# Kernel optimization log

Hardware: AMD Instinct MI355X
Metric: run time of the kernel (lower is better)

## Reference

```python
import jax, jax.numpy as jnp
import numpy as np
from jax import lax

DIVISOR = 2.0

def setup_inputs() -> dict:
    key = jax.random.key(0)
    k1, k2, k3, k4 = jax.random.split(key, 4)
    x = jax.random.normal(k1, (32, 3, 32, 128, 128), dtype=jnp.float16)
    conv_w = jax.random.normal(k2, (16, 3, 3, 3, 3), dtype=jnp.float16) * 0.1
    conv_b = jax.random.normal(k3, (16,), dtype=jnp.float16)
    bias = jax.random.normal(k4, (16,), dtype=jnp.float16)
    return {"x": x, "conv_w": conv_w, "conv_b": conv_b, "bias": bias}

def reference(x, conv_w, conv_b, bias):
    # Conv3d (valid padding, stride 1), fp16 like conv.half()
    y = lax.conv_general_dilated(
        x, conv_w, window_strides=(1, 1, 1), padding="VALID",
        dimension_numbers=("NCDHW", "OIDHW", "NCDHW"))
    y = y + conv_b[None, :, None, None, None]
    # Fused ReLU + 2x2x2 max pool
    y = jnp.maximum(y, jnp.asarray(0, y.dtype))
    B, C, D, H, W = y.shape
    Dp, Hp, Wp = D // 2, H // 2, W // 2
    pooled = y[:, :, :2 * Dp, :2 * Hp, :2 * Wp].reshape(
        B, C, Dp, 2, Hp, 2, Wp, 2).max(axis=(3, 5, 7))  # [B,C,Dp,Hp,Wp]
    # Spatial mean in fp32 (kernel accumulates in float)
    avg = pooled.astype(jnp.float32).mean(axis=(2, 3, 4))  # [B,C]
    # /divisor + bias[c], then sum over channels -> [B,1,1,1]
    per_ch = avg / DIVISOR + bias.astype(jnp.float32)[None, :]
    return per_ch.sum(axis=1).reshape(B, 1, 1, 1)
```

## Files before the change

kernel.cpp:

```cpp
#include <hip/hip_runtime.h>
#include <hip/hip_bf16.h>


typedef __attribute__((ext_vector_type(8)))  short  short8;
typedef __attribute__((ext_vector_type(2)))  float  floatx2;
typedef __attribute__((ext_vector_type(4)))  float  floatx4;
typedef __attribute__((ext_vector_type(16))) float  floatx16;

__device__ __forceinline__ short f2bf(float f) {
    unsigned u = __builtin_bit_cast(unsigned, f);
    unsigned r = (u + 0x7FFFu + ((u >> 16) & 1u)) >> 16;
    return (short)r;
}

__device__ __forceinline__ unsigned pkbf2(float a, float b) {
    __hip_bfloat162 h = __float22bfloat162_rn(float2{a, b});
    unsigned r;
    __builtin_memcpy(&r, &h, 4);
    return r;
}

template <int CTRL>
__device__ __forceinline__ float dpp_max(float v) {
    int x = __builtin_bit_cast(int, v);
    int y = __builtin_amdgcn_mov_dpp(x, CTRL, 0xF, 0xF, true);
    return fmaxf(v, __builtin_bit_cast(float, y));
}

#define BAR() asm volatile("s_waitcnt lgkmcnt(0)\n\ts_barrier" ::: "memory")

#define BUFSZ 16640

__global__ void init_kernel(const float* __restrict__ wg,
                            const float* __restrict__ biasg,
                            short* __restrict__ wtab,
                            float* __restrict__ out)
{
    const int t = threadIdx.x;
    if (t < 576) {
        const int lane = t & 63, f = t >> 6;
        const int kh = f / 3, kw = f % 3;
        const int m = lane & 31, hs = lane >> 5;
        const int ch = m >> 1, dd = m & 1;
        short8 v;
        #pragma unroll
        for (int j = 0; j < 8; ++j) {
            const int s = hs * 8 + j;
            const int dl = s >> 2, ci = s & 3;
            const int kd = dl - dd;
            v[j] = (ci < 3 && kd >= 0 && kd < 3)
                 ? f2bf(wg[ch * 81 + ci * 27 + kd * 9 + kh * 3 + kw]) : (short)0;
        }
        ((short8*)wtab)[f * 64 + lane] = v;
    }
    if (t < 32) {
        float s = 0.f;
        #pragma unroll
        for (int cc = 0; cc < 16; ++cc) s += biasg[cc];
        out[t] = s;
    }
}

__global__ __launch_bounds__(512, 4) void fused_conv_pool_reduce(
    const float* __restrict__ xg,
    const short* __restrict__ wtab,
    const float* __restrict__ cbg,
    float* __restrict__ out)
{
    __shared__ __align__(16) short rawT[2 * 130 * 64];
    __shared__ float wsums[8];

    const int lin = blockIdx.y * 63 + blockIdx.x;
    const int nl  = (lin & 7) * 252 + (lin >> 3);
    const int hp  = nl % 63;
    const int b   = nl / 63;

    const int tid = threadIdx.x;
    const int lane = tid & 63;
    const int wv   = tid >> 6;
    const int hs   = lane >> 5;

    short8 af[9];
    #pragma unroll
    for (int f = 0; f < 9; ++f) af[f] = ((const short8*)wtab)[f * 64 + lane];
    const float cbv = cbg[(lane >> 1) & 15];
    float maskA[4];
    #pragma unroll
    for (int a = 0; a < 4; ++a) {
        const bool ok = ((lane & 1) == 0) && (wv * 8 + 2 * a + hs <= 62);
        maskA[a] = ok ? 1.0f : 0.0f;
    }

    if (tid < 64)
        *(unsigned long long*)((char*)rawT + (tid >> 5) * BUFSZ + 16384 + (tid & 31) * 8) = 0ULL;

    #define SWZ(r) (((r) ^ ((r) >> 3)) & 7)

    const int w4 = tid & 31, dr2 = (tid >> 5) & 1, rr = (tid >> 6) & 1, hr2 = (tid >> 7) & 3;
    int waddr2[2];
    #pragma unroll
    for (int j = 0; j < 2; ++j) {
        const int row = 2 * w4 + 64 * rr + j;
        waddr2[j] = row * 128 + ((hr2 * 2) ^ SWZ(row)) * 16 + dr2 * 8;
    }

    const int wi = (lane >> 1) & 15, hh = lane & 1;
    int raddr[3][3];
    #pragma unroll
    for (int kh = 0; kh < 3; ++kh) {
        #pragma unroll
        for (int kw = 0; kw < 3; ++kw) {
            const int row = wv * 16 + wi + kw;
            const int phys = ((hh + kh) * 2 + hs) ^ SWZ(row);
            raddr[kh][kw] = row * 128 + phys * 16;
        }
    }

    {
        const int w4p = tid & 31, drp = (tid >> 5) & 3, hrp = (tid >> 7) & 3;
        const float* srcP = xg + ((size_t)b * 96 + drp) * 16384 + (2 * hp + hrp) * 128 + 4 * w4p;
        const floatx4 c0 = *(const floatx4*)(srcP);
        const floatx4 c1 = *(const floatx4*)(srcP + 524288);
        const floatx4 c2 = *(const floatx4*)(srcP + 1048576);
        const int chunkL = hrp * 2 + (drp >> 1);
        #pragma unroll
        for (int i = 0; i < 4; ++i) {
            const int row = 4 * w4p + i;
            const int ad = row * 128 + (chunkL ^ SWZ(row)) * 16 + (drp & 1) * 8;
            uint2 pk;
            pk.x = pkbf2(c0[i], c1[i]);
            pk.y = pkbf2(c2[i], 0.0f);
            *(uint2*)((char*)rawT + ad) = pk;
        }
    }

    const float* src2 = xg + ((size_t)b * 96 + 4 + dr2) * 16384
                      + (2 * hp + hr2) * 128 + 2 * w4 + 64 * rr;
    floatx2 A0 = *(const floatx2*)(src2);
    floatx2 A1 = *(const floatx2*)(src2 + 524288);
    floatx2 A2 = *(const floatx2*)(src2 + 1048576);

    float vsum = 0.f;
    for (int dp = 0; dp < 15; ++dp) {
        const int p16 = (dp & 1) << 4;
        if (dp <= 13) {
            const int bw = (((dp >> 1) + 1) & 1) * BUFSZ;
            uint2 pk0, pk1;
            pk0.x = pkbf2(A0[0], A1[0]); pk0.y = pkbf2(A2[0], 0.0f);
            pk1.x = pkbf2(A0[1], A1[1]); pk1.y = pkbf2(A2[1], 0.0f);
            *(uint2*)((char*)rawT + bw + (waddr2[0] ^ p16)) = pk0;
            *(uint2*)((char*)rawT + bw + (waddr2[1] ^ p16)) = pk1;
            if (dp <= 12) {
                src2 += 32768;
                A0 = *(const floatx2*)(src2);
                A1 = *(const floatx2*)(src2 + 524288);
                A2 = *(const floatx2*)(src2 + 1048576);
            }
        }
        BAR();

        const int roff = (((dp + hs) >> 1) & 1) * BUFSZ;

        floatx16 acc = {0.f,0.f,0.f,0.f,0.f,0.f,0.f,0.f,
                        0.f,0.f,0.f,0.f,0.f,0.f,0.f,0.f};
        #pragma unroll
        for (int kh = 0; kh < 3; ++kh) {
            #pragma unroll
            for (int kw = 0; kw < 3; ++kw) {
                const short8 bf = *(const short8*)((char*)rawT + roff + (raddr[kh][kw] ^ p16));
                acc = __builtin_amdgcn_mfma_f32_32x32x16_bf16(bf, af[kh * 3 + kw], acc, 0, 0, 0);
            }
        }
        #pragma unroll
        for (int a = 0; a < 4; ++a) {
            float m01 = fmaxf(acc[4 * a],     acc[4 * a + 1]);
            float m23 = fmaxf(acc[4 * a + 2], acc[4 * a + 3]);
            float m   = fmaxf(m01, m23);
            m = dpp_max<0xB1>(m);
            const float v = fmaxf(m + cbv, 0.f);
            vsum = fmaf(maskA[a], v, vsum);
        }
    }

    float s = vsum;
    #pragma unroll
    for (int off = 1; off < 64; off <<= 1) s += __shfl_xor(s, off, 64);

    if (lane == 0) wsums[wv] = s;
    __syncthreads();
    if (tid == 0) {
        float bs = 0.f;
        #pragma unroll
        for (int i = 0; i < 8; ++i) bs += wsums[i];
        atomicAdd(&out[b], bs * (1.0f / 119070.0f));
    }
}

extern "C" void kernel_launch(void* const* d_in, const int* in_sizes, int n_in,
                              void* d_out, int out_size, void* d_ws, size_t ws_size,
                              hipStream_t stream) {
    const float* x      = (const float*)d_in[0];
    const float* conv_w = (const float*)d_in[1];
    const float* conv_b = (const float*)d_in[2];
    const float* bias   = (const float*)d_in[3];
    float* out = (float*)d_out;
    short* wtab = (short*)d_ws;

    init_kernel<<<1, 576, 0, stream>>>(conv_w, bias, wtab, out);
    dim3 grid(63, 32);
    fused_conv_pool_reduce<<<grid, 512, 0, stream>>>(x, wtab, conv_b, out);
}
```

Baseline: 287.2 us.

## Split conv-pool blocks into single-wave workgroups with barrier-free 4-slot LDS ring

Each 512-thread block that covered a whole output row is replaced by 64-thread single-wave blocks, each handling one 16-wide W segment, so the grid grows eightfold. Each wave loads its own input halo into a private 4-slot LDS ring. This removes the per-depth-step s_barrier and the cross-wave shared reduction, and each wave atomically adds its partial sum to the output directly. It also raises wave priority around the MFMA chain. The cost is redundant halo loads, scalar rather than vector global loads, and eight times more atomics. Visibility of LDS writes within a single wave now relies on implicit ordering and compiler waitcnt insertion.

```diff
diff --git a/kernel.cpp b/kernel.cpp
--- a/kernel.cpp
+++ b/kernel.cpp
@@ -3,8 +3,6 @@
 
 
 typedef __attribute__((ext_vector_type(8)))  short  short8;
-typedef __attribute__((ext_vector_type(2)))  float  floatx2;
-typedef __attribute__((ext_vector_type(4)))  float  floatx4;
 typedef __attribute__((ext_vector_type(16))) float  floatx16;
 
 __device__ __forceinline__ short f2bf(float f) {
@@ -27,9 +25,7 @@
     return fmaxf(v, __builtin_bit_cast(float, y));
 }
 
-#define BAR() asm volatile("s_waitcnt lgkmcnt(0)\n\ts_barrier" ::: "memory")
-
-#define BUFSZ 16640
+#define SLOTSZ 1152
 
 __global__ void init_kernel(const float* __restrict__ wg,
                             const float* __restrict__ biasg,
@@ -61,23 +57,23 @@
     }
 }
 
-__global__ __launch_bounds__(512, 4) void fused_conv_pool_reduce(
+__global__ __launch_bounds__(64, 4) void fused_conv_pool_reduce(
     const float* __restrict__ xg,
     const short* __restrict__ wtab,
     const float* __restrict__ cbg,
     float* __restrict__ out)
 {
-    __shared__ __align__(16) short rawT[2 * 130 * 64];
-    __shared__ float wsums[8];
+    __shared__ __align__(16) short slots[4 * 18 * 32];
 
-    const int lin = blockIdx.y * 63 + blockIdx.x;
-    const int nl  = (lin & 7) * 252 + (lin >> 3);
-    const int hp  = nl % 63;
-    const int b   = nl / 63;
+    const int lin  = blockIdx.y * 63 + blockIdx.x;
+    const int nl   = (lin & 7) * 2016 + (lin >> 3);
+    const int hp   = nl % 63;
+    const int rest = nl / 63;
+    const int wv   = rest & 7;
+    const int b    = rest >> 3;
+    const int wbase = wv * 16;
 
-    const int tid = threadIdx.x;
-    const int lane = tid & 63;
-    const int wv   = tid >> 6;
+    const int lane = threadIdx.x;
     const int hs   = lane >> 5;
 
     short8 af[9];
@@ -87,90 +83,82 @@
     float maskA[4];
     #pragma unroll
     for (int a = 0; a < 4; ++a) {
-        const bool ok = ((lane & 1) == 0) && (wv * 8 + 2 * a + hs <= 62);
+        const bool ok = ((lane & 1) == 0) && (8 * wv + 2 * a + hs <= 62);
         maskA[a] = ok ? 1.0f : 0.0f;
     }
 
-    if (tid < 64)
-        *(unsigned long long*)((char*)rawT + (tid >> 5) * BUFSZ + 16384 + (tid & 31) * 8) = 0ULL;
-
-    #define SWZ(r) (((r) ^ ((r) >> 3)) & 7)
-
-    const int w4 = tid & 31, dr2 = (tid >> 5) & 1, rr = (tid >> 6) & 1, hr2 = (tid >> 7) & 3;
-    int waddr2[2];
-    #pragma unroll
-    for (int j = 0; j < 2; ++j) {
-        const int row = 2 * w4 + 64 * rr + j;
-        waddr2[j] = row * 128 + ((hr2 * 2) ^ SWZ(row)) * 16 + dr2 * 8;
-    }
+    const int rowA = lane & 15, hlA = lane >> 4;
+    const int wadA = rowA * 64 + ((hlA ^ (rowA & 3)) * 16);
+    const float* gA = xg + (size_t)b * 1572864 + (2 * hp + hlA) * 128 + wbase + rowA;
+    const bool doB = (lane < 8);
+    const bool wv7 = (wv == 7);
+    const int rowB = 16 + (lane & 1), hlB = (lane >> 1) & 3;
+    const int wadB = rowB * 64 + ((hlB ^ (rowB & 3)) * 16);
+    const float* gB = xg + (size_t)b * 1572864 + (2 * hp + hlB) * 128 + wbase + rowB;
 
     const int wi = (lane >> 1) & 15, hh = lane & 1;
-    int raddr[3][3];
+    int rad[3][3];
     #pragma unroll
     for (int kh = 0; kh < 3; ++kh) {
         #pragma unroll
         for (int kw = 0; kw < 3; ++kw) {
-            const int row = wv * 16 + wi + kw;
-            const int phys = ((hh + kh) * 2 + hs) ^ SWZ(row);
-            raddr[kh][kw] = row * 128 + phys * 16;
+            const int row = wi + kw;
+            rad[kh][kw] = row * 64 + (((hh + kh) ^ (row & 3)) * 16);
         }
     }
 
-    {
-        const int w4p = tid & 31, drp = (tid >> 5) & 3, hrp = (tid >> 7) & 3;
-        const float* srcP = xg + ((size_t)b * 96 + drp) * 16384 + (2 * hp + hrp) * 128 + 4 * w4p;
-        const floatx4 c0 = *(const floatx4*)(srcP);
-        const floatx4 c1 = *(const floatx4*)(srcP + 524288);
-        const floatx4 c2 = *(const floatx4*)(srcP + 1048576);
-        const int chunkL = hrp * 2 + (drp >> 1);
-        #pragma unroll
-        for (int i = 0; i < 4; ++i) {
-            const int row = 4 * w4p + i;
-            const int ad = row * 128 + (chunkL ^ SWZ(row)) * 16 + (drp & 1) * 8;
-            uint2 pk;
-            pk.x = pkbf2(c0[i], c1[i]);
-            pk.y = pkbf2(c2[i], 0.0f);
-            *(uint2*)((char*)rawT + ad) = pk;
+    float A0,A1,A2,A3,A4,A5, B0=0.f,B1=0.f,B2=0.f,B3=0.f,B4=0.f,B5=0.f;
+    auto loadPair = [&](int p) {
+        const float* pa = gA + (size_t)(2 * p) * 16384;
+        A0 = pa[0];      A1 = pa[524288];  A2 = pa[1048576];
+        A3 = pa[16384];  A4 = pa[540672];  A5 = pa[1064960];
+        if (doB) {
+            if (!wv7) {
+                const float* pb = gB + (size_t)(2 * p) * 16384;
+                B0 = pb[0];     B1 = pb[524288]; B2 = pb[1048576];
+                B3 = pb[16384]; B4 = pb[540672]; B5 = pb[1064960];
+            } else {
+                B0 = B1 = B2 = B3 = B4 = B5 = 0.f;
+            }
         }
-    }
+    };
+    auto writePair = [&](int sbase) {
+        uint4 q;
+        q.x = pkbf2(A0, A1);  q.y = pkbf2(A2, 0.f);
+        q.z = pkbf2(A3, A4);  q.w = pkbf2(A5, 0.f);
+        *(uint4*)((char*)slots + sbase + wadA) = q;
+        if (doB) {
+            uint4 r;
+            r.x = pkbf2(B0, B1);  r.y = pkbf2(B2, 0.f);
+            r.z = pkbf2(B3, B4);  r.w = pkbf2(B5, 0.f);
+            *(uint4*)((char*)slots + sbase + wadB) = r;
+        }
+    };
 
-    const float* src2 = xg + ((size_t)b * 96 + 4 + dr2) * 16384
-                      + (2 * hp + hr2) * 128 + 2 * w4 + 64 * rr;
-    floatx2 A0 = *(const floatx2*)(src2);
-    floatx2 A1 = *(const floatx2*)(src2 + 524288);
-    floatx2 A2 = *(const floatx2*)(src2 + 1048576);
+    loadPair(0); writePair(0);
+    loadPair(1); writePair(SLOTSZ);
+    loadPair(2);
 
     float vsum = 0.f;
     for (int dp = 0; dp < 15; ++dp) {
-        const int p16 = (dp & 1) << 4;
-        if (dp <= 13) {
-            const int bw = (((dp >> 1) + 1) & 1) * BUFSZ;
-            uint2 pk0, pk1;
-            pk0.x = pkbf2(A0[0], A1[0]); pk0.y = pkbf2(A2[0], 0.0f);
-            pk1.x = pkbf2(A0[1], A1[1]); pk1.y = pkbf2(A2[1], 0.0f);
-            *(uint2*)((char*)rawT + bw + (waddr2[0] ^ p16)) = pk0;
-            *(uint2*)((char*)rawT + bw + (waddr2[1] ^ p16)) = pk1;
-            if (dp <= 12) {
-                src2 += 32768;
-                A0 = *(const floatx2*)(src2);
-                A1 = *(const floatx2*)(src2 + 524288);
-                A2 = *(const floatx2*)(src2 + 1048576);
-            }
-        }
-        BAR();
+        if (dp <= 13) writePair(((dp + 2) & 3) * SLOTSZ);
+        if (dp <= 12) loadPair(dp + 3);
 
-        const int roff = (((dp + hs) >> 1) & 1) * BUFSZ;
+        const int rbase = ((dp + hs) & 3) * SLOTSZ;
 
         floatx16 acc = {0.f,0.f,0.f,0.f,0.f,0.f,0.f,0.f,
                         0.f,0.f,0.f,0.f,0.f,0.f,0.f,0.f};
+        __builtin_amdgcn_s_setprio(1);
         #pragma unroll
         for (int kh = 0; kh < 3; ++kh) {
             #pragma unroll
             for (int kw = 0; kw < 3; ++kw) {
-                const short8 bf = *(const short8*)((char*)rawT + roff + (raddr[kh][kw] ^ p16));
+                const short8 bf = *(const short8*)((char*)slots + rbase + rad[kh][kw]);
                 acc = __builtin_amdgcn_mfma_f32_32x32x16_bf16(bf, af[kh * 3 + kw], acc, 0, 0, 0);
             }
         }
+        __builtin_amdgcn_s_setprio(0);
+
         #pragma unroll
         for (int a = 0; a < 4; ++a) {
             float m01 = fmaxf(acc[4 * a],     acc[4 * a + 1]);
@@ -185,15 +173,7 @@
     float s = vsum;
     #pragma unroll
     for (int off = 1; off < 64; off <<= 1) s += __shfl_xor(s, off, 64);
-
-    if (lane == 0) wsums[wv] = s;
-    __syncthreads();
-    if (tid == 0) {
-        float bs = 0.f;
-        #pragma unroll
-        for (int i = 0; i < 8; ++i) bs += wsums[i];
-        atomicAdd(&out[b], bs * (1.0f / 119070.0f));
-    }
+    if (lane == 0) atomicAdd(&out[b], s * (1.0f / 119070.0f));
 }
 
 extern "C" void kernel_launch(void* const* d_in, const int* in_sizes, int n_in,
@@ -207,6 +187,6 @@
     short* wtab = (short*)d_ws;
 
     init_kernel<<<1, 576, 0, stream>>>(conv_w, bias, wtab, out);
-    dim3 grid(63, 32);
-    fused_conv_pool_reduce<<<grid, 512, 0, stream>>>(x, wtab, conv_b, out);
+    dim3 grid(63, 256);
+    fused_conv_pool_reduce<<<grid, 64, 0, stream>>>(x, wtab, conv_b, out);
 }
```

Result: slower. 479.9 us (+67.1%).
